# Optimization experiments

Hardware: AMD Instinct MI355X
Metric: run time of the kernel (lower is better)

## Reference

```python
import jax, jax.numpy as jnp
import numpy as np
from jax import lax

NUM_BINS = 8


def setup_inputs() -> dict:
    key = jax.random.key(0)
    kx, kc, kw = jax.random.split(key, 3)
    N, H, W, C = 8, 128, 128, 64
    x = jax.random.uniform(kx, (N, H, W, C), dtype=jnp.float32)
    # he_normal-style initializers for the learned tables
    co_matrix = jax.random.normal(kc, (NUM_BINS, NUM_BINS), dtype=jnp.float32) * np.sqrt(2.0 / NUM_BINS)
    w_spatial = jax.random.normal(kw, (3, 3), dtype=jnp.float32) * np.sqrt(2.0 / 9.0)
    return {"x": x, "co_matrix": co_matrix, "w_spatial": w_spatial}


def reference(x, co_matrix, w_spatial):
    """Co-occurrence layer: y(p) = sum_b co[bin(x_p), b] * conv(x * 1[bin(x)==b], w)(p).

    This is the vectorized form of the per-bin tf.while_loop in CoLL.call:
    quantize input into num_bins buckets, run the spatial filter on each
    bin-masked copy of x, then gather the co-occurrence row for each output
    element's bin and accumulate across bins.
    """
    num_bins = co_matrix.shape[0]
    N, H, W, C = x.shape
    k = w_spatial.shape[0]

    # --- quantization_input_as_bins: uniform bins over [min, max] ---
    xmin = jnp.min(x)
    xmax = jnp.max(x)
    scale = num_bins / (xmax - xmin + jnp.asarray(1e-8, x.dtype))
    idx = jnp.clip(jnp.floor((x - xmin) * scale), 0, num_bins - 1).astype(jnp.int32)  # [N,H,W,C]

    # --- per-bin masked copies of x: [N,H,W,C,B] -> fold into channels ---
    onehot = jax.nn.one_hot(idx, num_bins, dtype=x.dtype)           # [N,H,W,C,B]
    xb = (x[..., None] * onehot).reshape(N, H, W, C * num_bins)     # [N,H,W,C*B]

    # --- shared spatial filter applied depthwise to every (channel, bin) slice ---
    kern = jnp.broadcast_to(w_spatial[:, :, None, None], (k, k, 1, C * num_bins))  # HWIO depthwise
    z = lax.conv_general_dilated(
        xb, kern,
        window_strides=(1, 1), padding="SAME",
        dimension_numbers=("NHWC", "HWIO", "NHWC"),
        feature_group_count=C * num_bins,
    ).reshape(N, H, W, C, num_bins)                                  # [N,H,W,C,B]

    # --- gather co-occurrence row by the output element's bin, accumulate ---
    co_rows = co_matrix[idx]                                         # [N,H,W,C,B]
    y = jnp.sum(co_rows * z, axis=-1)                                # [N,H,W,C]
    return y
```

## Files before the change

### kernel.cpp

```cpp
#include <hip/hip_runtime.h>


static constexpr int IMG4 = 128 * 128 * 16;
static constexpr int NBLK = 1024, NTHR = 256;

__device__ __forceinline__ int qbin(float v, float xmin, float scale) {
    float t = (v - xmin) * scale;
    t = fminf(t, 7.0f);
    return (int)t;
}

__global__ __launch_bounds__(256) void reduce_k(const float4* __restrict__ x4,
                                                float2* __restrict__ part) {
    const int ofs = blockIdx.x * 256 + threadIdx.x;
    float4 v[8];
#pragma unroll
    for (int k = 0; k < 8; ++k) v[k] = x4[k * IMG4 + ofs];

    float lmin = v[0].x, lmax = v[0].x;
#pragma unroll
    for (int k = 0; k < 8; ++k) {
        lmin = fminf(lmin, fminf(fminf(v[k].x, v[k].y), fminf(v[k].z, v[k].w)));
        lmax = fmaxf(lmax, fmaxf(fmaxf(v[k].x, v[k].y), fmaxf(v[k].z, v[k].w)));
    }
#pragma unroll
    for (int off = 32; off; off >>= 1) {
        lmin = fminf(lmin, __shfl_xor(lmin, off, 64));
        lmax = fmaxf(lmax, __shfl_xor(lmax, off, 64));
    }
    __shared__ float smin[4], smax[4];
    const int wid = threadIdx.x >> 6, lane = threadIdx.x & 63;
    if (lane == 0) { smin[wid] = lmin; smax[wid] = lmax; }
    __syncthreads();
    if (threadIdx.x == 0) {
        part[blockIdx.x] = make_float2(
            fminf(fminf(smin[0], smin[1]), fminf(smin[2], smin[3])),
            fmaxf(fmaxf(smax[0], smax[1]), fmaxf(smax[2], smax[3])));
    }
}

__global__ __launch_bounds__(256) void coll_k(const float4* __restrict__ x4,
                                              const float* __restrict__ co,
                                              const float* __restrict__ wsp,
                                              float4* __restrict__ y4,
                                              const float2* __restrict__ part) {
    __shared__ float co_s[64], w_s[9];
    __shared__ float cw[9 * 64];
    __shared__ float sred[8];

    if (threadIdx.x < 64) co_s[threadIdx.x] = co[threadIdx.x];
    if (threadIdx.x < 9)  w_s[threadIdx.x] = wsp[threadIdx.x];

    float gmin = 3.4028235e38f, gmax = -3.4028235e38f;
#pragma unroll
    for (int j = 0; j < 4; ++j) {
        float2 p = part[threadIdx.x * 4 + j];
        gmin = fminf(gmin, p.x);
        gmax = fmaxf(gmax, p.y);
    }
#pragma unroll
    for (int off = 32; off; off >>= 1) {
        gmin = fminf(gmin, __shfl_xor(gmin, off, 64));
        gmax = fmaxf(gmax, __shfl_xor(gmax, off, 64));
    }
    const int wid = threadIdx.x >> 6, lane = threadIdx.x & 63;
    if (lane == 0) { sred[wid] = gmin; sred[4 + wid] = gmax; }
    __syncthreads();

    for (int idx = threadIdx.x; idx < 576; idx += 256)
        cw[idx] = w_s[idx >> 6] * co_s[idx & 63];

    const float xmin = fminf(fminf(sred[0], sred[1]), fminf(sred[2], sred[3]));
    const float xmax = fmaxf(fmaxf(sred[4], sred[5]), fmaxf(sred[6], sred[7]));
    const float scale = 8.0f / ((xmax - xmin) + 1e-8f);
    __syncthreads();

    const int ofs = blockIdx.x * 256 + threadIdx.x;
    const int w = (ofs >> 4) & 127;
    const int h = (ofs >> 11) & 127;
    const bool wm = (w > 0), wp = (w < 127), hm = (h > 0), hp = (h < 127);

#pragma unroll 2
    for (int k = 0; k < 8; ++k) {
        const int base = k * IMG4 + ofs;
        const float4 xc = x4[base];
        const int bx = qbin(xc.x, xmin, scale), ipx = bx * 8;
        const int by = qbin(xc.y, xmin, scale), ipy = by * 8;
        const int bz = qbin(xc.z, xmin, scale), ipz = bz * 8;
        const int bw = qbin(xc.w, xmin, scale), ipw = bw * 8;

        float ax = xc.x * cw[4 * 64 + ipx + bx];
        float ay = xc.y * cw[4 * 64 + ipy + by];
        float az = xc.z * cw[4 * 64 + ipz + bz];
        float aw = xc.w * cw[4 * 64 + ipw + bw];

#define TAP(T, OFF) { \
        const float4 q = x4[base + (OFF)]; \
        ax = fmaf(q.x, cw[(T) * 64 + ipx + qbin(q.x, xmin, scale)], ax); \
        ay = fmaf(q.y, cw[(T) * 64 + ipy + qbin(q.y, xmin, scale)], ay); \
        az = fmaf(q.z, cw[(T) * 64 + ipz + qbin(q.z, xmin, scale)], az); \
        aw = fmaf(q.w, cw[(T) * 64 + ipw + qbin(q.w, xmin, scale)], aw); }

        if (hm && wm) TAP(0, -2064)
        if (hm)       TAP(1, -2048)
        if (hm && wp) TAP(2, -2032)
        if (wm)       TAP(3, -16)
        if (wp)       TAP(5,  16)
        if (hp && wm) TAP(6,  2032)
        if (hp)       TAP(7,  2048)
        if (hp && wp) TAP(8,  2064)
#undef TAP

        y4[base] = make_float4(ax, ay, az, aw);
    }
}

extern "C" void kernel_launch(void* const* d_in, const int* in_sizes, int n_in,
                              void* d_out, int out_size, void* d_ws, size_t ws_size,
                              hipStream_t stream) {
    const float4* x4 = (const float4*)d_in[0];
    const float*  co = (const float*)d_in[1];
    const float*  wsp = (const float*)d_in[2];
    float4* y4 = (float4*)d_out;
    float2* part = (float2*)d_ws;

    hipLaunchKernelGGL(reduce_k, dim3(NBLK), dim3(NTHR), 0, stream, x4, part);
    hipLaunchKernelGGL(coll_k, dim3(NBLK), dim3(NTHR), 0, stream,
                       x4, co, wsp, y4, part);
}
```

Measured before the change: 109.9 us.

## Fuse min/max reduction and co-occurrence conv into one kernel with grid barrier

Merges the two kernels into one persistent-style kernel: each block reduces its min/max, publishes it via order-preserving unsigned atomics into 32 grouped counters, and spins until all blocks have arrived. Afterwards it reads the global extrema and reuses the centre values already held in registers instead of reloading them. This removes a kernel launch boundary and one pass of centre loads. In exchange it adds a memset and a software grid barrier, which depends on all 1024 blocks being co-resident (launch_bounds 256,4 over the CUs). If they are not, the spin loop falls back to a bounded timeout and the result may be wrong.

```diff
diff --git a/kernel.cpp b/kernel.cpp
--- a/kernel.cpp
+++ b/kernel.cpp
@@ -3,19 +3,46 @@
 
 static constexpr int IMG4 = 128 * 128 * 16;
 static constexpr int NBLK = 1024, NTHR = 256;
+static constexpr int GROUPS = 32;
+static constexpr int ARRIVALS = NBLK / GROUPS;
+static constexpr int LSTRIDE = 32;
+static constexpr unsigned CNT_TARGET = 0xFFFFFFFFu - (unsigned)ARRIVALS;
 
+__device__ __forceinline__ unsigned f2key(float f) {
+    unsigned u = __float_as_uint(f);
+    return (u & 0x80000000u) ? ~u : (u | 0x80000000u);
+}
+__device__ __forceinline__ float key2f(unsigned k) {
+    unsigned u = (k & 0x80000000u) ? (k & 0x7FFFFFFFu) : ~k;
+    return __uint_as_float(u);
+}
 __device__ __forceinline__ int qbin(float v, float xmin, float scale) {
     float t = (v - xmin) * scale;
     t = fminf(t, 7.0f);
     return (int)t;
 }
 
-__global__ __launch_bounds__(256) void reduce_k(const float4* __restrict__ x4,
-                                                float2* __restrict__ part) {
+__global__ __launch_bounds__(256, 4) void fused_k(
+        const float4* __restrict__ x4, const float* __restrict__ co,
+        const float* __restrict__ wsp, float4* __restrict__ y4,
+        unsigned* __restrict__ ws) {
+
+    __shared__ float co_s[64], w_s[9], cw[9 * 64];
+    __shared__ float sred[8];
+    __shared__ unsigned skey[64];
+
     const int ofs = blockIdx.x * 256 + threadIdx.x;
+    const int wid = threadIdx.x >> 6, lane = threadIdx.x & 63;
+
     float4 v[8];
 #pragma unroll
     for (int k = 0; k < 8; ++k) v[k] = x4[k * IMG4 + ofs];
+
+    if (threadIdx.x < 64) co_s[threadIdx.x] = co[threadIdx.x];
+    if (threadIdx.x < 9)  w_s[threadIdx.x] = wsp[threadIdx.x];
+    __syncthreads();
+    for (int idx = threadIdx.x; idx < 576; idx += 256)
+        cw[idx] = w_s[idx >> 6] * co_s[idx & 63];
 
     float lmin = v[0].x, lmax = v[0].x;
 #pragma unroll
@@ -28,54 +55,49 @@
         lmin = fminf(lmin, __shfl_xor(lmin, off, 64));
         lmax = fmaxf(lmax, __shfl_xor(lmax, off, 64));
     }
-    __shared__ float smin[4], smax[4];
-    const int wid = threadIdx.x >> 6, lane = threadIdx.x & 63;
-    if (lane == 0) { smin[wid] = lmin; smax[wid] = lmax; }
-    __syncthreads();
-    if (threadIdx.x == 0) {
-        part[blockIdx.x] = make_float2(
-            fminf(fminf(smin[0], smin[1]), fminf(smin[2], smin[3])),
-            fmaxf(fmaxf(smax[0], smax[1]), fmaxf(smax[2], smax[3])));
-    }
-}
-
-__global__ __launch_bounds__(256) void coll_k(const float4* __restrict__ x4,
-                                              const float* __restrict__ co,
-                                              const float* __restrict__ wsp,
-                                              float4* __restrict__ y4,
-                                              const float2* __restrict__ part) {
-    __shared__ float co_s[64], w_s[9];
-    __shared__ float cw[9 * 64];
-    __shared__ float sred[8];
-
-    if (threadIdx.x < 64) co_s[threadIdx.x] = co[threadIdx.x];
-    if (threadIdx.x < 9)  w_s[threadIdx.x] = wsp[threadIdx.x];
-
-    float gmin = 3.4028235e38f, gmax = -3.4028235e38f;
-#pragma unroll
-    for (int j = 0; j < 4; ++j) {
-        float2 p = part[threadIdx.x * 4 + j];
-        gmin = fminf(gmin, p.x);
-        gmax = fmaxf(gmax, p.y);
-    }
-#pragma unroll
-    for (int off = 32; off; off >>= 1) {
-        gmin = fminf(gmin, __shfl_xor(gmin, off, 64));
-        gmax = fmaxf(gmax, __shfl_xor(gmax, off, 64));
-    }
-    const int wid = threadIdx.x >> 6, lane = threadIdx.x & 63;
-    if (lane == 0) { sred[wid] = gmin; sred[4 + wid] = gmax; }
+    if (lane == 0) { sred[wid] = lmin; sred[4 + wid] = lmax; }
     __syncthreads();
 
-    for (int idx = threadIdx.x; idx < 576; idx += 256)
-        cw[idx] = w_s[idx >> 6] * co_s[idx & 63];
+    const int g = blockIdx.x & (GROUPS - 1);
+    if (threadIdx.x == 0) {
+        float bmin = fminf(fminf(sred[0], sred[1]), fminf(sred[2], sred[3]));
+        float bmax = fmaxf(fmaxf(sred[4], sred[5]), fmaxf(sred[6], sred[7]));
+        atomicMin(&ws[g * LSTRIDE], f2key(bmin));
+        atomicMin(&ws[1024 + g * LSTRIDE], ~f2key(bmax));
+        __threadfence();
+        atomicSub(&ws[2048 + g * LSTRIDE], 1u);
+    }
 
-    const float xmin = fminf(fminf(sred[0], sred[1]), fminf(sred[2], sred[3]));
-    const float xmax = fmaxf(fmaxf(sred[4], sred[5]), fmaxf(sred[6], sred[7]));
-    const float scale = 8.0f / ((xmax - xmin) + 1e-8f);
+    if (threadIdx.x < 32) {
+        unsigned spins = 0;
+        while (__hip_atomic_load(&ws[2048 + threadIdx.x * LSTRIDE],
+                                 __ATOMIC_RELAXED, __HIP_MEMORY_SCOPE_AGENT)
+                   != CNT_TARGET &&
+               spins < (1u << 26)) ++spins;
+    }
+    __threadfence();
     __syncthreads();
 
-    const int ofs = blockIdx.x * 256 + threadIdx.x;
+    if (threadIdx.x < 32) {
+        skey[threadIdx.x] = __hip_atomic_load(&ws[threadIdx.x * LSTRIDE],
+                                              __ATOMIC_RELAXED,
+                                              __HIP_MEMORY_SCOPE_AGENT);
+        skey[32 + threadIdx.x] = __hip_atomic_load(&ws[1024 + threadIdx.x * LSTRIDE],
+                                                   __ATOMIC_RELAXED,
+                                                   __HIP_MEMORY_SCOPE_AGENT);
+    }
+    __syncthreads();
+
+    unsigned mk = skey[0], nk = skey[32];
+#pragma unroll
+    for (int i = 1; i < 32; ++i) {
+        mk = min(mk, skey[i]);
+        nk = min(nk, skey[32 + i]);
+    }
+    const float xmin = key2f(mk);
+    const float xmax = key2f(~nk);
+    const float scale = 8.0f / ((xmax - xmin) + 1e-8f);
+
     const int w = (ofs >> 4) & 127;
     const int h = (ofs >> 11) & 127;
     const bool wm = (w > 0), wp = (w < 127), hm = (h > 0), hp = (h < 127);
@@ -83,7 +105,7 @@
 #pragma unroll 2
     for (int k = 0; k < 8; ++k) {
         const int base = k * IMG4 + ofs;
-        const float4 xc = x4[base];
+        const float4 xc = v[k];
         const int bx = qbin(xc.x, xmin, scale), ipx = bx * 8;
         const int by = qbin(xc.y, xmin, scale), ipy = by * 8;
         const int bz = qbin(xc.z, xmin, scale), ipz = bz * 8;
@@ -122,9 +144,9 @@
     const float*  co = (const float*)d_in[1];
     const float*  wsp = (const float*)d_in[2];
     float4* y4 = (float4*)d_out;
-    float2* part = (float2*)d_ws;
+    unsigned* ws = (unsigned*)d_ws;
 
-    hipLaunchKernelGGL(reduce_k, dim3(NBLK), dim3(NTHR), 0, stream, x4, part);
-    hipLaunchKernelGGL(coll_k, dim3(NBLK), dim3(NTHR), 0, stream,
-                       x4, co, wsp, y4, part);
+    hipMemsetAsync(d_ws, 0xFF, 3 * 1024 * sizeof(unsigned), stream);
+    hipLaunchKernelGGL(fused_k, dim3(NBLK), dim3(NTHR), 0, stream,
+                       x4, co, wsp, y4, ws);
 }
```

New measurement: 264.5 us. +140.7%, slower.
